# Kernel tuning notes

Hardware: AMD Instinct MI355X
Metric: run time of the kernel (lower is better)

Reference implementation:

```python
import jax, jax.numpy as jnp
import numpy as np

# model dims
VOCAB = 32000; D = 256; FF = 1024; L = 2; NH = 8; HD_ATT = D // NH; T_MAX = 128
# memory bank dims
SLOTS = 512; MD = 128; MH = 4; HD = MD // MH; TOPK = 8
B = 4; T = 128


def _ln(x, g, b):
    m = x.mean(-1, keepdims=True)
    v = x.var(-1, keepdims=True)
    return (x - m) * jax.lax.rsqrt(v + 1e-5) * g + b


def _topk_softmax(scores, k):
    # sparse addressing: softmax restricted to the top-k slots per head
    vals = jax.lax.top_k(scores, k)[0]
    thr = vals[..., -1:]
    neg = jnp.finfo(scores.dtype).min
    return jax.nn.softmax(jnp.where(scores >= thr, scores, neg), axis=-1)


def setup_inputs() -> dict:
    key = jax.random.key(0)
    ks = jax.random.split(key, 12)
    s = 0.02
    return {
        "input_seq": jax.random.randint(ks[0], (B, T), 0, VOCAB),
        "tok_emb": jax.random.normal(ks[1], (VOCAB, D)) * s,
        "pos_emb": jax.random.normal(ks[2], (T_MAX, D)) * s,
        "Wqkv": jax.random.normal(ks[3], (L, D, 3 * D)) * s,
        "Wo": jax.random.normal(ks[4], (L, D, D)) * s,
        "ln1_g": jnp.ones((L, D)), "ln1_b": jnp.zeros((L, D)),
        "ln2_g": jnp.ones((L, D)), "ln2_b": jnp.zeros((L, D)),
        "W1": jax.random.normal(ks[5], (L, D, FF)) * s, "b1": jnp.zeros((L, FF)),
        "W2": jax.random.normal(ks[6], (L, FF, D)) * s, "b2": jnp.zeros((L, D)),
        "lnf_g": jnp.ones((D,)), "lnf_b": jnp.zeros((D,)),
        "W_logits": jax.random.normal(ks[7], (D + MD, VOCAB)) * s,
        "b_logits": jnp.zeros((VOCAB,)),
        "W_iface": jax.random.normal(ks[8], (D + MD, MH * (4 * HD + 1))) * s,
        "b_iface": jnp.zeros((MH * (4 * HD + 1),)),
        "beta_read": jnp.asarray(1.0), "beta_write": jnp.asarray(1.0),
    }


def _forward(input_seq, tok_emb, pos_emb, Wqkv, Wo, ln1_g, ln1_b, ln2_g, ln2_b,
             W1, b1, W2, b2, lnf_g, lnf_b, W_logits, b_logits, W_iface, b_iface,
             beta_read, beta_write):
    Bc, Tc = input_seq.shape
    x = tok_emb[input_seq] + pos_emb[:Tc]  # [B,T,D]
    neg = jnp.finfo(x.dtype).min
    causal = jnp.tril(jnp.ones((Tc, Tc), bool))
    for l in range(L):  # small fixed layer count
        h = _ln(x, ln1_g[l], ln1_b[l])
        q, k, v = jnp.split(h @ Wqkv[l], 3, axis=-1)
        q = q.reshape(Bc, Tc, NH, HD_ATT)
        k = k.reshape(Bc, Tc, NH, HD_ATT)
        v = v.reshape(Bc, Tc, NH, HD_ATT)
        att = jnp.einsum('bqhd,bkhd->bhqk', q, k) / np.sqrt(HD_ATT)
        att = jax.nn.softmax(jnp.where(causal, att, neg), axis=-1)
        o = jnp.einsum('bhqk,bkhd->bqhd', att, v).reshape(Bc, Tc, D)
        x = x + o @ Wo[l]
        h = _ln(x, ln2_g[l], ln2_b[l])
        x = x + jax.nn.gelu(h @ W1[l] + b1[l]) @ W2[l] + b2[l]
    x = _ln(x, lnf_g, lnf_b)  # causal controller states h_t for every prefix

    beta_r = jnp.clip(jax.nn.softplus(beta_read), 1.0, 20.0)
    beta_w = jnp.clip(jax.nn.softplus(beta_write), 1.0, 20.0)
    M0 = jnp.zeros((Bc, MH, SLOTS, HD), x.dtype)
    rv0 = jnp.zeros((Bc, MD), x.dtype)

    def step(carry, h_t):
        M, rv = carry
        c = jnp.concatenate([h_t, rv], axis=-1)  # [B, D+MD]
        logits_t = c @ W_logits + b_logits
        iface = (c @ W_iface + b_iface).reshape(Bc, MH, 4 * HD + 1)
        rk = iface[..., 0 * HD:1 * HD]
        wk = iface[..., 1 * HD:2 * HD]
        wv = iface[..., 2 * HD:3 * HD]
        erase = jax.nn.sigmoid(iface[..., 3 * HD:4 * HD])
        add_gate = jax.nn.sigmoid(iface[..., 4 * HD:])  # [B,MH,1]
        # read (topk content addressing), accumulate into read_vec
        w_r = _topk_softmax(jnp.einsum('bhd,bhsd->bhs', rk, M) * beta_r, TOPK)
        rv = rv + jnp.einsum('bhs,bhsd->bhd', w_r, M).reshape(Bc, MD)
        # write with erase/add gating
        w_w = _topk_softmax(jnp.einsum('bhd,bhsd->bhs', wk, M) * beta_w, TOPK)
        M = M * (1.0 - w_w[..., None] * erase[:, :, None, :]) \
            + (add_gate * w_w)[..., None] * wv[:, :, None, :]
        return (M, rv), logits_t

    _, logits = jax.lax.scan(step, (M0, rv0), jnp.swapaxes(x, 0, 1))
    return jnp.swapaxes(logits, 0, 1)  # [B,T,VOCAB]


def reference(input_seq, tok_emb, pos_emb, Wqkv, Wo, ln1_g, ln1_b, ln2_g, ln2_b,
              W1, b1, W2, b2, lnf_g, lnf_b, W_logits, b_logits, W_iface, b_iface,
              beta_read, beta_write):
    return _forward(input_seq, tok_emb, pos_emb, Wqkv, Wo, ln1_g, ln1_b, ln2_g,
                    ln2_b, W1, b1, W2, b2, lnf_g, lnf_b, W_logits, b_logits,
                    W_iface, b_iface, beta_read, beta_write)
```

## Files before the change

### kernel.cpp

```cpp
#include <hip/hip_runtime.h>
#include <hip/hip_bf16.h>
#include <math.h>

typedef __bf16 bf16;
typedef __bf16 bf16x8 __attribute__((ext_vector_type(8)));
typedef float f32x4 __attribute__((ext_vector_type(4)));
typedef float f32x16 __attribute__((ext_vector_type(16)));

#define B_ 4
#define T_ 128
#define D_ 256
#define FF_ 1024
#define HD_ 32
#define VOCAB_ 32000
#define NC_ 516
#define KBIG_ 384

struct TJob { const float* src; bf16* dst; int K; int N; int blk0; };
struct TJobs { TJob j[9]; };
__global__ __launch_bounds__(256) void k_tr_embed(TJobs js, const int* __restrict__ ids,
                                                  const float* __restrict__ tok,
                                                  const float* __restrict__ pos,
                                                  const float* __restrict__ g,
                                                  const float* __restrict__ b,
                                                  float* __restrict__ X, bf16* __restrict__ out) {
    int bid = blockIdx.x;
    if (bid < 420) {
        __shared__ float tile[64][65];
        int r = 0;
#pragma unroll
        for (int i = 1; i < 9; i++) if (bid >= js.j[i].blk0) r = i;
        TJob jb = js.j[r];
        int local = bid - jb.blk0;
        int tiles_k = jb.K >> 6;
        int ik = local % tiles_k, in = local / tiles_k;
        int k0 = ik * 64, n0 = in * 64;
        int tx = threadIdx.x & 63, ty = threadIdx.x >> 6;
#pragma unroll
        for (int rr = 0; rr < 64; rr += 4) {
            int kk = k0 + rr + ty, nn = n0 + tx;
            tile[rr + ty][tx] = (nn < jb.N) ? jb.src[(size_t)kk * jb.N + nn] : 0.f;
        }
        __syncthreads();
#pragma unroll
        for (int rr = 0; rr < 64; rr += 4) {
            int nn = n0 + rr + ty, kk = k0 + tx;
            jb.dst[(size_t)nn * jb.K + kk] = (bf16)tile[tx][rr + ty];
        }
        return;
    }
    int row = bid - 420;
    int d   = threadIdx.x;
    int t   = row & (T_ - 1);
    int id  = ids[row];
    float v = tok[(size_t)id * D_ + d] + pos[(size_t)t * D_ + d];
    X[(size_t)row * D_ + d] = v;
    float s1 = v, s2 = v * v;
#pragma unroll
    for (int off = 32; off > 0; off >>= 1) {
        s1 += __shfl_xor(s1, off);
        s2 += __shfl_xor(s2, off);
    }
    __shared__ float r1[4], r2[4];
    int wid = d >> 6, lane = d & 63;
    if (lane == 0) { r1[wid] = s1; r2[wid] = s2; }
    __syncthreads();
    float tot1 = r1[0] + r1[1] + r1[2] + r1[3];
    float tot2 = r2[0] + r2[1] + r2[2] + r2[3];
    float mean = tot1 * (1.f / D_);
    float var  = tot2 * (1.f / D_) - mean * mean;
    float rs   = rsqrtf(var + 1e-5f);
    out[(size_t)row * D_ + d] = (bf16)((v - mean) * rs * g[d] + b[d]);
}

__global__ void k_ln(const float* __restrict__ X, const float* __restrict__ g,
                     const float* __restrict__ b, bf16* __restrict__ out, int ostride) {
    int row = blockIdx.x;
    int d   = threadIdx.x;
    float v = X[(size_t)row * D_ + d];
    float s1 = v, s2 = v * v;
#pragma unroll
    for (int off = 32; off > 0; off >>= 1) {
        s1 += __shfl_xor(s1, off);
        s2 += __shfl_xor(s2, off);
    }
    __shared__ float r1[4], r2[4];
    int wid = d >> 6, lane = d & 63;
    if (lane == 0) { r1[wid] = s1; r2[wid] = s2; }
    __syncthreads();
    float tot1 = r1[0] + r1[1] + r1[2] + r1[3];
    float tot2 = r2[0] + r2[1] + r2[2] + r2[3];
    float mean = tot1 * (1.f / D_);
    float var  = tot2 * (1.f / D_) - mean * mean;
    float rs   = rsqrtf(var + 1e-5f);
    out[(size_t)row * ostride + d] = (bf16)((v - mean) * rs * g[d] + b[d]);
}

template <bool BIAS, bool GELU_, bool RESID, bool OBF16>
__global__ __launch_bounds__(256) void k_dgemm(const bf16* __restrict__ A, int lda,
                                               const bf16* __restrict__ BT,
                                               const float* __restrict__ bias,
                                               float* __restrict__ Cf, bf16* __restrict__ Cb,
                                               int ldc, int N, int K) {
    int tid = threadIdx.x;
    int lane = tid & 63, wid = tid >> 6;
    int wm = wid >> 1, wn = wid & 1;
    int m0 = blockIdx.y * 64, n0 = blockIdx.x * 64;
    int r = lane & 15, q = lane >> 4;

    const bf16* Ab = A  + (size_t)(m0 + wm * 32 + r) * lda + q * 8;
    const bf16* Bb = BT + (size_t)(n0 + wn * 32 + r) * K   + q * 8;

    f32x4 acc[2][2] = {};
#pragma unroll 4
    for (int k0 = 0; k0 < K; k0 += 32) {
        bf16x8 a0 = *(const bf16x8*)(Ab + k0);
        bf16x8 a1 = *(const bf16x8*)(Ab + (size_t)16 * lda + k0);
        bf16x8 b0 = *(const bf16x8*)(Bb + k0);
        bf16x8 b1 = *(const bf16x8*)(Bb + (size_t)16 * K + k0);
        acc[0][0] = __builtin_amdgcn_mfma_f32_16x16x32_bf16(a0, b0, acc[0][0], 0, 0, 0);
        acc[0][1] = __builtin_amdgcn_mfma_f32_16x16x32_bf16(a0, b1, acc[0][1], 0, 0, 0);
        acc[1][0] = __builtin_amdgcn_mfma_f32_16x16x32_bf16(a1, b0, acc[1][0], 0, 0, 0);
        acc[1][1] = __builtin_amdgcn_mfma_f32_16x16x32_bf16(a1, b1, acc[1][1], 0, 0, 0);
    }

#pragma unroll
    for (int mi = 0; mi < 2; mi++) {
#pragma unroll
        for (int ni = 0; ni < 2; ni++) {
            int col = n0 + wn * 32 + ni * 16 + r;
            if (col < N) {
                int rowb = m0 + wm * 32 + mi * 16 + (q << 2);
                float bsv = BIAS ? bias[col] : 0.f;
#pragma unroll
                for (int j = 0; j < 4; j++) {
                    float val = acc[mi][ni][j] + bsv;
                    if (GELU_) {
                        float u = val;
                        val = 0.5f * u * (1.f + tanhf(0.7978845608028654f * (u + 0.044715f * u * u * u)));
                    }
                    size_t idx = (size_t)(rowb + j) * ldc + col;
                    if (RESID) Cf[idx] += val;
                    else if (OBF16) Cb[idx] = (bf16)val;
                    else Cf[idx] = val;
                }
            }
        }
    }
}

__global__ __launch_bounds__(256) void k_logits(const bf16* __restrict__ A,
                                                const float* __restrict__ Bm,
                                                const float* __restrict__ bias,
                                                float* __restrict__ C) {
    __shared__ __align__(16) bf16 BsT[64][392];
    int tid = threadIdx.x;
    int lane = tid & 63, wid = tid >> 6;
    int wm = wid >> 1, wn = wid & 1;
    int n0 = blockIdx.x * 64;

    int bn = tid & 63, bk = (tid >> 6) << 3;
#pragma unroll
    for (int k0 = 0; k0 < KBIG_; k0 += 32) {
        bf16x8 bv;
#pragma unroll
        for (int e = 0; e < 8; e++) bv[e] = (bf16)Bm[(size_t)(k0 + bk + e) * VOCAB_ + n0 + bn];
        *(bf16x8*)&BsT[bn][k0 + bk] = bv;
    }
    __syncthreads();

    float bsv[2];
#pragma unroll
    for (int ni = 0; ni < 2; ni++) bsv[ni] = bias[n0 + wn * 32 + ni * 16 + (lane & 15)];

    int kfrag = (lane >> 4) << 3;
    for (int mt = 0; mt < 8; mt++) {
        int m0 = mt * 64;
        f32x4 acc[2][2] = {};
#pragma unroll
        for (int kk = 0; kk < KBIG_; kk += 32) {
            bf16x8 af[2], bfv[2];
#pragma unroll
            for (int mi = 0; mi < 2; mi++)
                af[mi] = *(const bf16x8*)&A[(size_t)(m0 + wm * 32 + mi * 16 + (lane & 15)) * KBIG_ + kk + kfrag];
#pragma unroll
            for (int ni = 0; ni < 2; ni++)
                bfv[ni] = *(const bf16x8*)&BsT[wn * 32 + ni * 16 + (lane & 15)][kk + kfrag];
#pragma unroll
            for (int mi = 0; mi < 2; mi++)
#pragma unroll
                for (int ni = 0; ni < 2; ni++)
                    acc[mi][ni] = __builtin_amdgcn_mfma_f32_16x16x32_bf16(af[mi], bfv[ni], acc[mi][ni], 0, 0, 0);
        }
#pragma unroll
        for (int mi = 0; mi < 2; mi++) {
#pragma unroll
            for (int ni = 0; ni < 2; ni++) {
                int colg = n0 + wn * 32 + ni * 16 + (lane & 15);
                int rowb = m0 + wm * 32 + mi * 16 + ((lane >> 4) << 2);
#pragma unroll
                for (int j = 0; j < 4; j++)
                    C[(size_t)(rowb + j) * VOCAB_ + colg] = acc[mi][ni][j] + bsv[ni];
            }
        }
    }
}

__global__ __launch_bounds__(256) void k_attn(const float* __restrict__ QKV, bf16* __restrict__ O) {
    __shared__ __align__(16) bf16 Qs[128][40];
    __shared__ __align__(16) bf16 Ks[128][40];
    __shared__ __align__(16) bf16 VT[32][136];
    __shared__ __align__(16) bf16 PT[128][136];
    __shared__ float Ls[128];
    int tid = threadIdx.x;
    int lane = tid & 63, w = tid >> 6;
    int l5 = lane >> 5, l31 = lane & 31;
    int b = blockIdx.x >> 3, h = blockIdx.x & 7;

    {
        int t = tid & 127, half = tid >> 7, d0 = half * 16;
        size_t rowb = (size_t)(b * T_ + t) * 768 + h * HD_ + d0;
        bf16 tq[16], tk[16];
#pragma unroll
        for (int i4 = 0; i4 < 4; i4++) {
            float4 qv = *(const float4*)&QKV[rowb + 4 * i4];
            float4 kv = *(const float4*)&QKV[rowb + 256 + 4 * i4];
            float4 vv = *(const float4*)&QKV[rowb + 512 + 4 * i4];
            tq[4 * i4] = (bf16)qv.x; tq[4 * i4 + 1] = (bf16)qv.y; tq[4 * i4 + 2] = (bf16)qv.z; tq[4 * i4 + 3] = (bf16)qv.w;
            tk[4 * i4] = (bf16)kv.x; tk[4 * i4 + 1] = (bf16)kv.y; tk[4 * i4 + 2] = (bf16)kv.z; tk[4 * i4 + 3] = (bf16)kv.w;
            VT[d0 + 4 * i4][t]     = (bf16)vv.x;
            VT[d0 + 4 * i4 + 1][t] = (bf16)vv.y;
            VT[d0 + 4 * i4 + 2][t] = (bf16)vv.z;
            VT[d0 + 4 * i4 + 3][t] = (bf16)vv.w;
        }
        *(bf16x8*)&Qs[t][d0]     = *(bf16x8*)&tq[0];
        *(bf16x8*)&Qs[t][d0 + 8] = *(bf16x8*)&tq[8];
        *(bf16x8*)&Ks[t][d0]     = *(bf16x8*)&tk[0];
        *(bf16x8*)&Ks[t][d0 + 8] = *(bf16x8*)&tk[8];
    }
    __syncthreads();

    const float scale = 0.17677669529663687f;
#pragma unroll
    for (int qt = 0; qt < 4; qt++) {
        f32x16 acc = {};
        bf16x8 a0 = *(const bf16x8*)&Ks[32 * w + l31][8 * l5];
        bf16x8 b0 = *(const bf16x8*)&Qs[32 * qt + l31][8 * l5];
        acc = __builtin_amdgcn_mfma_f32_32x32x16_bf16(a0, b0, acc, 0, 0, 0);
        bf16x8 a1 = *(const bf16x8*)&Ks[32 * w + l31][16 + 8 * l5];
        bf16x8 b1 = *(const bf16x8*)&Qs[32 * qt + l31][16 + 8 * l5];
        acc = __builtin_amdgcn_mfma_f32_32x32x16_bf16(a1, b1, acc, 0, 0, 0);
        int qg = 32 * qt + l31;
#pragma unroll
        for (int r = 0; r < 16; r++) {
            int key = 32 * w + (r & 3) + 8 * (r >> 2) + 4 * l5;
            float p = (key <= qg) ? expf(acc[r] * scale) : 0.f;
            PT[qg][key] = (bf16)p;
        }
    }
    __syncthreads();

    if (tid < 128) {
        float s = 0.f;
#pragma unroll
        for (int kk = 0; kk < 128; kk += 8) {
            bf16x8 v = *(const bf16x8*)&PT[tid][kk];
#pragma unroll
            for (int j = 0; j < 8; j++) s += (float)v[j];
        }
        Ls[tid] = 1.f / s;
    }

    f32x16 oacc = {};
#pragma unroll
    for (int kap = 0; kap < 8; kap++) {
        bf16x8 af = *(const bf16x8*)&PT[32 * w + l31][16 * kap + 8 * l5];
        bf16x8 bv = *(const bf16x8*)&VT[l31][16 * kap + 8 * l5];
        oacc = __builtin_amdgcn_mfma_f32_32x32x16_bf16(af, bv, oacc, 0, 0, 0);
    }
    __syncthreads();
#pragma unroll
    for (int r = 0; r < 16; r++) {
        int qg = 32 * w + (r & 3) + 8 * (r >> 2) + 4 * l5;
        O[(size_t)(b * T_ + qg) * D_ + h * HD_ + l31] = (bf16)(oacc[r] * Ls[qg]);
    }
}

__global__ __launch_bounds__(256) void k_scan(const float* __restrict__ Wif,
                                              const float* __restrict__ HIF,
                                              bf16* __restrict__ Abig) {
    int b = blockIdx.x, tid = threadIdx.x;
    int lane = tid & 63, w = tid >> 6;
    int r = lane & 15, q = lane >> 4;
    int d = lane & 31;

    __shared__ bf16 hifc[T_][264];
    __shared__ bf16 rvh[T_][128];
    __shared__ __align__(16) bf16 rvb[2][128];

    bf16x8 bfrag[5][4];
#pragma unroll
    for (int ti = 0; ti < 5; ti++) {
#pragma unroll
        for (int kap = 0; kap < 4; kap++) {
            bf16x8 v;
#pragma unroll
            for (int j = 0; j < 8; j++) {
                int k = 32 * kap + 8 * q + j;
                float wv_ = 0.f;
                if (ti < 4) {
                    int fl = w * 129 + 64 + 16 * ti + r;
                    wv_ = Wif[(size_t)(256 + k) * NC_ + fl];
                } else if (r == 0) {
                    wv_ = Wif[(size_t)(256 + k) * NC_ + (w * 129 + 128)];
                }
                v[j] = (bf16)wv_;
            }
            bfrag[ti][kap] = v;
        }
    }

    for (int idx = tid; idx < T_ * 260; idx += 256) {
        int t  = idx / 260;
        int cc = idx - t * 260;
        int fl = (cc < 256) ? ((cc >> 6) * 129 + 64 + (cc & 63)) : ((cc - 256) * 129 + 128);
        hifc[t][cc] = (bf16)HIF[(size_t)(b * T_ + t) * NC_ + fl];
    }
    if (tid < 128) rvb[0][tid] = (bf16)0.f;
    float rv1 = 0.f, mm1 = 0.f;
    __syncthreads();

    for (int t = 0; t < T_; t++) {
        const bf16* rb = &rvb[t & 1][0];
        bf16x8 afr0 = *(const bf16x8*)&rb[8 * q];
        bf16x8 afr1 = *(const bf16x8*)&rb[32 + 8 * q];
        bf16x8 afr2 = *(const bf16x8*)&rb[64 + 8 * q];
        bf16x8 afr3 = *(const bf16x8*)&rb[96 + 8 * q];

        float tv[5];
#pragma unroll
        for (int ti = 0; ti < 5; ti++) {
            f32x4 a0 = {}, a1 = {};
            a0 = __builtin_amdgcn_mfma_f32_16x16x32_bf16(afr0, bfrag[ti][0], a0, 0, 0, 0);
            a1 = __builtin_amdgcn_mfma_f32_16x16x32_bf16(afr1, bfrag[ti][1], a1, 0, 0, 0);
            a0 = __builtin_amdgcn_mfma_f32_16x16x32_bf16(afr2, bfrag[ti][2], a0, 0, 0, 0);
            a1 = __builtin_amdgcn_mfma_f32_16x16x32_bf16(afr3, bfrag[ti][3], a1, 0, 0, 0);
            tv[ti] = a0[0] + a1[0];
        }
        float wv0 = __shfl(tv[0], r), wv1 = __shfl(tv[1], r);
        float er0 = __shfl(tv[2], r), er1 = __shfl(tv[3], r);
        float gv  = __shfl(tv[4], 0);
        float gw = (d < 16) ? wv0 : wv1;
        float ge = (d < 16) ? er0 : er1;

        if (lane < 32) {
            float gwv = gw + (float)hifc[t][64 * w + d];
            float gev = ge + (float)hifc[t][64 * w + 32 + d];
            float gav = gv + (float)hifc[t][256 + w];
            float er = 1.f / (1.f + expf(-gev));
            float ag = 1.f / (1.f + expf(-gav));
            rvh[t][32 * w + d] = (bf16)rv1;
            float mn = mm1 * (1.f - er * (1.f / 512.f)) + ag * (1.f / 512.f) * gwv;
            rv1 += mm1;
            mm1 = mn;
            rvb[(t + 1) & 1][32 * w + d] = (bf16)rv1;
        }
        __syncthreads();
    }

    for (int idx = tid; idx < T_ * 128; idx += 256) {
        int t = idx >> 7, dd = idx & 127;
        Abig[(size_t)(b * T_ + t) * KBIG_ + 256 + dd] = rvh[t][dd];
    }
}

extern "C" void kernel_launch(void* const* d_in, const int* in_sizes, int n_in,
                              void* d_out, int out_size, void* d_ws, size_t ws_size,
                              hipStream_t stream) {
    const int*   ids  = (const int*)d_in[0];
    const float* tok  = (const float*)d_in[1];
    const float* pos  = (const float*)d_in[2];
    const float* Wqkv = (const float*)d_in[3];
    const float* Wo   = (const float*)d_in[4];
    const float* ln1g = (const float*)d_in[5];
    const float* ln1b = (const float*)d_in[6];
    const float* ln2g = (const float*)d_in[7];
    const float* ln2b = (const float*)d_in[8];
    const float* W1   = (const float*)d_in[9];
    const float* b1   = (const float*)d_in[10];
    const float* W2   = (const float*)d_in[11];
    const float* b2   = (const float*)d_in[12];
    const float* lnfg = (const float*)d_in[13];
    const float* lnfb = (const float*)d_in[14];
    const float* Wl   = (const float*)d_in[15];
    const float* bl   = (const float*)d_in[16];
    const float* Wif  = (const float*)d_in[17];
    const float* bif  = (const float*)d_in[18];

    char* ws = (char*)d_ws;
    float* X    = (float*)(ws + 0);
    float* QKV  = (float*)(ws + 524288);
    bf16*  Hb   = (bf16*)(ws + 2097152);
    bf16*  Obf  = (bf16*)(ws + 2359296);
    bf16*  FF1  = (bf16*)(ws + 2621440);
    float* HIF  = (float*)(ws + 3670016);
    bf16*  Abig = (bf16*)(ws + 4726784);
    bf16*  WqkvT= (bf16*)(ws + 5120000);
    bf16*  WoT  = (bf16*)(ws + 5906432);
    bf16*  W1T  = (bf16*)(ws + 6168576);
    bf16*  W2T  = (bf16*)(ws + 7217152);
    bf16*  WifT = (bf16*)(ws + 8265728);
    float* outp = (float*)d_out;

    TJobs js;
    int blk = 0;
    auto setj = [&](int i, const float* s, bf16* d, int K, int N, int Npad) {
        js.j[i] = {s, d, K, N, blk};
        blk += (K >> 6) * (Npad >> 6);
    };
    setj(0, Wqkv,              WqkvT,              256, 768, 768);
    setj(1, Wqkv + 256 * 768,  WqkvT + 768 * 256,  256, 768, 768);
    setj(2, Wo,                WoT,                256, 256, 256);
    setj(3, Wo + 256 * 256,    WoT + 256 * 256,    256, 256, 256);
    setj(4, W1,                W1T,                256, 1024, 1024);
    setj(5, W1 + 256 * 1024,   W1T + 1024 * 256,   256, 1024, 1024);
    setj(6, W2,                W2T,                1024, 256, 256);
    setj(7, W2 + 1024 * 256,   W2T + 256 * 1024,   1024, 256, 256);
    setj(8, Wif,               WifT,               256, NC_, 576);

    k_tr_embed<<<blk + 512, 256, 0, stream>>>(js, ids, tok, pos, ln1g, ln1b, X, Hb);

    for (int l = 0; l < 2; l++) {
        k_dgemm<false, false, false, false><<<dim3(12, 8), 256, 0, stream>>>(
            Hb, D_, WqkvT + (size_t)l * 768 * 256, nullptr, QKV, nullptr, 768, 768, 256);
        k_attn<<<32, 256, 0, stream>>>(QKV, Obf);
        k_dgemm<false, false, true, false><<<dim3(4, 8), 256, 0, stream>>>(
            Obf, D_, WoT + (size_t)l * 256 * 256, nullptr, X, nullptr, D_, D_, 256);
        k_ln<<<512, 256, 0, stream>>>(X, ln2g + l * D_, ln2b + l * D_, Hb, D_);
        k_dgemm<true, true, false, true><<<dim3(16, 8), 256, 0, stream>>>(
            Hb, D_, W1T + (size_t)l * 1024 * 256, b1 + l * FF_, nullptr, FF1, FF_, FF_, 256);
        k_dgemm<true, false, true, false><<<dim3(4, 8), 256, 0, stream>>>(
            FF1, FF_, W2T + (size_t)l * 256 * 1024, b2 + l * D_, X, nullptr, D_, D_, 1024);
        if (l == 0)
            k_ln<<<512, 256, 0, stream>>>(X, ln1g + D_, ln1b + D_, Hb, D_);
    }

    k_ln<<<512, 256, 0, stream>>>(X, lnfg, lnfb, Abig, KBIG_);
    k_dgemm<true, false, false, false><<<dim3(9, 8), 256, 0, stream>>>(
        Abig, KBIG_, WifT, bif, HIF, nullptr, NC_, NC_, 256);
    k_scan<<<4, 256, 0, stream>>>(Wif, HIF, Abig);
    k_logits<<<500, 256, 0, stream>>>(Abig, Wl, bl, outp);
}
```

Measured before the change: 278.6 us.

## Fuse memory scan and logits kernels with flag-based inter-block sync

Merges the 4-block sequential memory scan and the 500-block logits GEMM into one launch. Logits blocks stage their W_logits tile into shared memory, then spin on a global counter until the scan blocks publish the read vectors, so the weight loading overlaps the serial scan. The scan also stops staging all HIF columns into shared memory and instead prefetches the next timestep's values into registers. The cost is spin-waiting, plus a reliance on the four scan blocks being scheduled alongside the waiting ones, which risks deadlock if they are not.

```diff
diff --git a/kernel.cpp b/kernel.cpp
--- a/kernel.cpp
+++ b/kernel.cpp
@@ -23,8 +23,10 @@
                                                   const float* __restrict__ pos,
                                                   const float* __restrict__ g,
                                                   const float* __restrict__ b,
-                                                  float* __restrict__ X, bf16* __restrict__ out) {
+                                                  float* __restrict__ X, bf16* __restrict__ out,
+                                                  unsigned* __restrict__ flags) {
     int bid = blockIdx.x;
+    if (bid == 0 && threadIdx.x == 0) flags[0] = 0u;
     if (bid < 420) {
         __shared__ float tile[64][65];
         int r = 0;
@@ -149,63 +151,6 @@
     }
 }
 
-__global__ __launch_bounds__(256) void k_logits(const bf16* __restrict__ A,
-                                                const float* __restrict__ Bm,
-                                                const float* __restrict__ bias,
-                                                float* __restrict__ C) {
-    __shared__ __align__(16) bf16 BsT[64][392];
-    int tid = threadIdx.x;
-    int lane = tid & 63, wid = tid >> 6;
-    int wm = wid >> 1, wn = wid & 1;
-    int n0 = blockIdx.x * 64;
-
-    int bn = tid & 63, bk = (tid >> 6) << 3;
-#pragma unroll
-    for (int k0 = 0; k0 < KBIG_; k0 += 32) {
-        bf16x8 bv;
-#pragma unroll
-        for (int e = 0; e < 8; e++) bv[e] = (bf16)Bm[(size_t)(k0 + bk + e) * VOCAB_ + n0 + bn];
-        *(bf16x8*)&BsT[bn][k0 + bk] = bv;
-    }
-    __syncthreads();
-
-    float bsv[2];
-#pragma unroll
-    for (int ni = 0; ni < 2; ni++) bsv[ni] = bias[n0 + wn * 32 + ni * 16 + (lane & 15)];
-
-    int kfrag = (lane >> 4) << 3;
-    for (int mt = 0; mt < 8; mt++) {
-        int m0 = mt * 64;
-        f32x4 acc[2][2] = {};
-#pragma unroll
-        for (int kk = 0; kk < KBIG_; kk += 32) {
-            bf16x8 af[2], bfv[2];
-#pragma unroll
-            for (int mi = 0; mi < 2; mi++)
-                af[mi] = *(const bf16x8*)&A[(size_t)(m0 + wm * 32 + mi * 16 + (lane & 15)) * KBIG_ + kk + kfrag];
-#pragma unroll
-            for (int ni = 0; ni < 2; ni++)
-                bfv[ni] = *(const bf16x8*)&BsT[wn * 32 + ni * 16 + (lane & 15)][kk + kfrag];
-#pragma unroll
-            for (int mi = 0; mi < 2; mi++)
-#pragma unroll
-                for (int ni = 0; ni < 2; ni++)
-                    acc[mi][ni] = __builtin_amdgcn_mfma_f32_16x16x32_bf16(af[mi], bfv[ni], acc[mi][ni], 0, 0, 0);
-        }
-#pragma unroll
-        for (int mi = 0; mi < 2; mi++) {
-#pragma unroll
-            for (int ni = 0; ni < 2; ni++) {
-                int colg = n0 + wn * 32 + ni * 16 + (lane & 15);
-                int rowb = m0 + wm * 32 + mi * 16 + ((lane >> 4) << 2);
-#pragma unroll
-                for (int j = 0; j < 4; j++)
-                    C[(size_t)(rowb + j) * VOCAB_ + colg] = acc[mi][ni][j] + bsv[ni];
-            }
-        }
-    }
-}
-
 __global__ __launch_bounds__(256) void k_attn(const float* __restrict__ QKV, bf16* __restrict__ O) {
     __shared__ __align__(16) bf16 Qs[128][40];
     __shared__ __align__(16) bf16 Ks[128][40];
@@ -286,91 +231,163 @@
     }
 }
 
-__global__ __launch_bounds__(256) void k_scan(const float* __restrict__ Wif,
-                                              const float* __restrict__ HIF,
-                                              bf16* __restrict__ Abig) {
-    int b = blockIdx.x, tid = threadIdx.x;
+union SPool {
+    struct { bf16 rvh[T_][128]; __align__(16) bf16 rvb[2][128]; } scan;
+    struct { __align__(16) bf16 BsT[64][392]; } log;
+};
+
+__global__ __launch_bounds__(256) void k_scan_logits(const float* __restrict__ Wif,
+                                                     const float* __restrict__ HIF,
+                                                     bf16* __restrict__ Abig,
+                                                     const float* __restrict__ Bm,
+                                                     const float* __restrict__ bias,
+                                                     float* __restrict__ C,
+                                                     unsigned* __restrict__ flags) {
+    __shared__ SPool sp;
+    int tid = threadIdx.x;
     int lane = tid & 63, w = tid >> 6;
-    int r = lane & 15, q = lane >> 4;
-    int d = lane & 31;
-
-    __shared__ bf16 hifc[T_][264];
-    __shared__ bf16 rvh[T_][128];
-    __shared__ __align__(16) bf16 rvb[2][128];
-
-    bf16x8 bfrag[5][4];
-#pragma unroll
-    for (int ti = 0; ti < 5; ti++) {
-#pragma unroll
-        for (int kap = 0; kap < 4; kap++) {
-            bf16x8 v;
-#pragma unroll
-            for (int j = 0; j < 8; j++) {
-                int k = 32 * kap + 8 * q + j;
-                float wv_ = 0.f;
-                if (ti < 4) {
-                    int fl = w * 129 + 64 + 16 * ti + r;
-                    wv_ = Wif[(size_t)(256 + k) * NC_ + fl];
-                } else if (r == 0) {
-                    wv_ = Wif[(size_t)(256 + k) * NC_ + (w * 129 + 128)];
+
+    if (blockIdx.x < 4) {
+        int b = blockIdx.x;
+        int r = lane & 15, q = lane >> 4;
+        int d = lane & 31;
+
+        bf16x8 bfrag[5][4];
+#pragma unroll
+        for (int ti = 0; ti < 5; ti++) {
+#pragma unroll
+            for (int kap = 0; kap < 4; kap++) {
+                bf16x8 v;
+#pragma unroll
+                for (int j = 0; j < 8; j++) {
+                    int k = 32 * kap + 8 * q + j;
+                    float wv_ = 0.f;
+                    if (ti < 4) {
+                        int fl = w * 129 + 64 + 16 * ti + r;
+                        wv_ = Wif[(size_t)(256 + k) * NC_ + fl];
+                    } else if (r == 0) {
+                        wv_ = Wif[(size_t)(256 + k) * NC_ + (w * 129 + 128)];
+                    }
+                    v[j] = (bf16)wv_;
                 }
-                v[j] = (bf16)wv_;
-            }
-            bfrag[ti][kap] = v;
-        }
-    }
-
-    for (int idx = tid; idx < T_ * 260; idx += 256) {
-        int t  = idx / 260;
-        int cc = idx - t * 260;
-        int fl = (cc < 256) ? ((cc >> 6) * 129 + 64 + (cc & 63)) : ((cc - 256) * 129 + 128);
-        hifc[t][cc] = (bf16)HIF[(size_t)(b * T_ + t) * NC_ + fl];
-    }
-    if (tid < 128) rvb[0][tid] = (bf16)0.f;
-    float rv1 = 0.f, mm1 = 0.f;
-    __syncthreads();
-
-    for (int t = 0; t < T_; t++) {
-        const bf16* rb = &rvb[t & 1][0];
-        bf16x8 afr0 = *(const bf16x8*)&rb[8 * q];
-        bf16x8 afr1 = *(const bf16x8*)&rb[32 + 8 * q];
-        bf16x8 afr2 = *(const bf16x8*)&rb[64 + 8 * q];
-        bf16x8 afr3 = *(const bf16x8*)&rb[96 + 8 * q];
-
-        float tv[5];
-#pragma unroll
-        for (int ti = 0; ti < 5; ti++) {
-            f32x4 a0 = {}, a1 = {};
-            a0 = __builtin_amdgcn_mfma_f32_16x16x32_bf16(afr0, bfrag[ti][0], a0, 0, 0, 0);
-            a1 = __builtin_amdgcn_mfma_f32_16x16x32_bf16(afr1, bfrag[ti][1], a1, 0, 0, 0);
-            a0 = __builtin_amdgcn_mfma_f32_16x16x32_bf16(afr2, bfrag[ti][2], a0, 0, 0, 0);
-            a1 = __builtin_amdgcn_mfma_f32_16x16x32_bf16(afr3, bfrag[ti][3], a1, 0, 0, 0);
-            tv[ti] = a0[0] + a1[0];
-        }
-        float wv0 = __shfl(tv[0], r), wv1 = __shfl(tv[1], r);
-        float er0 = __shfl(tv[2], r), er1 = __shfl(tv[3], r);
-        float gv  = __shfl(tv[4], 0);
-        float gw = (d < 16) ? wv0 : wv1;
-        float ge = (d < 16) ? er0 : er1;
-
-        if (lane < 32) {
-            float gwv = gw + (float)hifc[t][64 * w + d];
-            float gev = ge + (float)hifc[t][64 * w + 32 + d];
-            float gav = gv + (float)hifc[t][256 + w];
-            float er = 1.f / (1.f + expf(-gev));
-            float ag = 1.f / (1.f + expf(-gav));
-            rvh[t][32 * w + d] = (bf16)rv1;
-            float mn = mm1 * (1.f - er * (1.f / 512.f)) + ag * (1.f / 512.f) * gwv;
-            rv1 += mm1;
-            mm1 = mn;
-            rvb[(t + 1) & 1][32 * w + d] = (bf16)rv1;
-        }
+                bfrag[ti][kap] = v;
+            }
+        }
+
+        const float* HB = HIF + (size_t)(b * T_) * NC_ + w * 129;
+        float hw_n = HB[64 + d], he_n = HB[96 + d], ha_n = HB[128];
+
+        if (tid < 128) sp.scan.rvb[0][tid] = (bf16)0.f;
+        float rv1 = 0.f, mm1 = 0.f;
         __syncthreads();
-    }
-
-    for (int idx = tid; idx < T_ * 128; idx += 256) {
-        int t = idx >> 7, dd = idx & 127;
-        Abig[(size_t)(b * T_ + t) * KBIG_ + 256 + dd] = rvh[t][dd];
+
+        for (int t = 0; t < T_; t++) {
+            const bf16* rb = &sp.scan.rvb[t & 1][0];
+            bf16x8 afr0 = *(const bf16x8*)&rb[8 * q];
+            bf16x8 afr1 = *(const bf16x8*)&rb[32 + 8 * q];
+            bf16x8 afr2 = *(const bf16x8*)&rb[64 + 8 * q];
+            bf16x8 afr3 = *(const bf16x8*)&rb[96 + 8 * q];
+
+            float hw = hw_n, he = he_n, ha = ha_n;
+            if (t + 1 < T_) {
+                const float* Hr = HB + (size_t)(t + 1) * NC_;
+                hw_n = Hr[64 + d]; he_n = Hr[96 + d]; ha_n = Hr[128];
+            }
+
+            float tv[5];
+#pragma unroll
+            for (int ti = 0; ti < 5; ti++) {
+                f32x4 a0 = {}, a1 = {};
+                a0 = __builtin_amdgcn_mfma_f32_16x16x32_bf16(afr0, bfrag[ti][0], a0, 0, 0, 0);
+                a1 = __builtin_amdgcn_mfma_f32_16x16x32_bf16(afr1, bfrag[ti][1], a1, 0, 0, 0);
+                a0 = __builtin_amdgcn_mfma_f32_16x16x32_bf16(afr2, bfrag[ti][2], a0, 0, 0, 0);
+                a1 = __builtin_amdgcn_mfma_f32_16x16x32_bf16(afr3, bfrag[ti][3], a1, 0, 0, 0);
+                tv[ti] = a0[0] + a1[0];
+            }
+            float wv0 = __shfl(tv[0], r), wv1 = __shfl(tv[1], r);
+            float er0 = __shfl(tv[2], r), er1 = __shfl(tv[3], r);
+            float gv  = __shfl(tv[4], 0);
+            float gw = (d < 16) ? wv0 : wv1;
+            float ge = (d < 16) ? er0 : er1;
+
+            if (lane < 32) {
+                float gwv = gw + hw;
+                float gev = ge + he;
+                float gav = gv + ha;
+                float er = 1.f / (1.f + expf(-gev));
+                float ag = 1.f / (1.f + expf(-gav));
+                sp.scan.rvh[t][32 * w + d] = (bf16)rv1;
+                float mn = mm1 * (1.f - er * (1.f / 512.f)) + ag * (1.f / 512.f) * gwv;
+                rv1 += mm1;
+                mm1 = mn;
+                sp.scan.rvb[(t + 1) & 1][32 * w + d] = (bf16)rv1;
+            }
+            __syncthreads();
+        }
+
+        for (int idx = tid; idx < T_ * 128; idx += 256) {
+            int t = idx >> 7, dd = idx & 127;
+            Abig[(size_t)(b * T_ + t) * KBIG_ + 256 + dd] = sp.scan.rvh[t][dd];
+        }
+        __threadfence();
+        __syncthreads();
+        if (tid == 0) atomicAdd(&flags[0], 1u);
+        return;
+    }
+
+    int wm = w >> 1, wn = w & 1;
+    int n0 = (blockIdx.x - 4) * 64;
+
+    int bn = tid & 63, bk = (tid >> 6) << 3;
+#pragma unroll
+    for (int k0 = 0; k0 < KBIG_; k0 += 32) {
+        bf16x8 bv;
+#pragma unroll
+        for (int e = 0; e < 8; e++) bv[e] = (bf16)Bm[(size_t)(k0 + bk + e) * VOCAB_ + n0 + bn];
+        *(bf16x8*)&sp.log.BsT[bn][k0 + bk] = bv;
+    }
+
+    float bsv[2];
+#pragma unroll
+    for (int ni = 0; ni < 2; ni++) bsv[ni] = bias[n0 + wn * 32 + ni * 16 + (lane & 15)];
+
+    if (tid == 0) {
+        while (atomicAdd(&flags[0], 0u) < 4u) __builtin_amdgcn_s_sleep(32);
+    }
+    __syncthreads();
+    __threadfence();
+
+    const bf16* A = Abig;
+    int kfrag = (lane >> 4) << 3;
+    for (int mt = 0; mt < 8; mt++) {
+        int m0 = mt * 64;
+        f32x4 acc[2][2] = {};
+#pragma unroll
+        for (int kk = 0; kk < KBIG_; kk += 32) {
+            bf16x8 af[2], bfv[2];
+#pragma unroll
+            for (int mi = 0; mi < 2; mi++)
+                af[mi] = *(const bf16x8*)&A[(size_t)(m0 + wm * 32 + mi * 16 + (lane & 15)) * KBIG_ + kk + kfrag];
+#pragma unroll
+            for (int ni = 0; ni < 2; ni++)
+                bfv[ni] = *(const bf16x8*)&sp.log.BsT[wn * 32 + ni * 16 + (lane & 15)][kk + kfrag];
+#pragma unroll
+            for (int mi = 0; mi < 2; mi++)
+#pragma unroll
+                for (int ni = 0; ni < 2; ni++)
+                    acc[mi][ni] = __builtin_amdgcn_mfma_f32_16x16x32_bf16(af[mi], bfv[ni], acc[mi][ni], 0, 0, 0);
+        }
+#pragma unroll
+        for (int mi = 0; mi < 2; mi++) {
+#pragma unroll
+            for (int ni = 0; ni < 2; ni++) {
+                int colg = n0 + wn * 32 + ni * 16 + (lane & 15);
+                int rowb = m0 + wm * 32 + mi * 16 + ((lane >> 4) << 2);
+#pragma unroll
+                for (int j = 0; j < 4; j++)
+                    C[(size_t)(rowb + j) * VOCAB_ + colg] = acc[mi][ni][j] + bsv[ni];
+            }
+        }
     }
 }
 
@@ -410,6 +427,7 @@
     bf16*  W1T  = (bf16*)(ws + 6168576);
     bf16*  W2T  = (bf16*)(ws + 7217152);
     bf16*  WifT = (bf16*)(ws + 8265728);
+    unsigned* flags = (unsigned*)(ws + 8560640);
     float* outp = (float*)d_out;
 
     TJobs js;
@@ -428,7 +446,7 @@
     setj(7, W2 + 1024 * 256,   W2T + 256 * 1024,   1024, 256, 256);
     setj(8, Wif,               WifT,               256, NC_, 576);
 
-    k_tr_embed<<<blk + 512, 256, 0, stream>>>(js, ids, tok, pos, ln1g, ln1b, X, Hb);
+    k_tr_embed<<<blk + 512, 256, 0, stream>>>(js, ids, tok, pos, ln1g, ln1b, X, Hb, flags);
 
     for (int l = 0; l < 2; l++) {
         k_dgemm<false, false, false, false><<<dim3(12, 8), 256, 0, stream>>>(
@@ -448,6 +466,5 @@
     k_ln<<<512, 256, 0, stream>>>(X, lnfg, lnfb, Abig, KBIG_);
     k_dgemm<true, false, false, false><<<dim3(9, 8), 256, 0, stream>>>(
         Abig, KBIG_, WifT, bif, HIF, nullptr, NC_, NC_, 256);
-    k_scan<<<4, 256, 0, stream>>>(Wif, HIF, Abig);
-    k_logits<<<500, 256, 0, stream>>>(Abig, Wl, bl, outp);
-}
+    k_scan_logits<<<504, 256, 0, stream>>>(Wif, HIF, Abig, Wl, bl, outp, flags);
+}
```

Result: no change. 283.1 us (+1.6%).
